# Kernel tuning notes

Hardware: AMD Instinct MI355X
Metric: run time of the kernel (lower is better)

Reference implementation:

```python
import jax, jax.numpy as jnp
import numpy as np

LAYERS, DIM, FFN, HEADS = 2, 1024, 4096, 8
HD = DIM // HEADS          # head qk dim = 128
VD = DIM                   # v_dim (double_v_dim=False)
HV = VD // HEADS           # head v dim = 128
B, L = 2, 2048
SCALE_BASE = 512.0
EPS = 1e-5


def setup_inputs() -> dict:
    key = jax.random.key(0)
    ks = jax.random.split(key, 18)
    def rn(k, shape, s=1.0):
        return jax.random.normal(k, shape, dtype=jnp.float32) * s
    return dict(
        X=rn(ks[0], (B, L, DIM)),
        Wq=rn(ks[1], (LAYERS, HEADS, DIM, HD), 1.0 / DIM),
        Wk=rn(ks[2], (LAYERS, HEADS, DIM, HD), 1.0 / DIM),
        Wv=rn(ks[3], (LAYERS, HEADS, DIM, HV), 1.0 / DIM),
        W_G=rn(ks[4], (LAYERS, DIM, VD), 1.0 / DIM),
        W_O=rn(ks[5], (LAYERS, VD, DIM), 1.0 / DIM),
        gn_w=1.0 + 0.02 * rn(ks[6], (LAYERS, VD)),
        gn_b=0.02 * rn(ks[7], (LAYERS, VD)),
        ln1_w=1.0 + 0.02 * rn(ks[8], (LAYERS, DIM)),
        ln1_b=0.02 * rn(ks[9], (LAYERS, DIM)),
        ln2_w=1.0 + 0.02 * rn(ks[10], (LAYERS, DIM)),
        ln2_b=0.02 * rn(ks[11], (LAYERS, DIM)),
        ffn_w1=rn(ks[12], (LAYERS, DIM, FFN), DIM ** -0.5),
        ffn_b1=0.02 * rn(ks[13], (LAYERS, FFN)),
        ffn_w2=rn(ks[14], (LAYERS, FFN, DIM), FFN ** -0.5),
        ffn_b2=0.02 * rn(ks[15], (LAYERS, DIM)),
    )


def _xpos_tables(length, head_dim):
    half = head_dim // 2
    pos = jnp.arange(length, dtype=jnp.float32)
    base_scale = (jnp.arange(0, head_dim, 2, dtype=jnp.float32) + 0.4 * head_dim) / (1.4 * head_dim)
    sc = base_scale[None, :] ** (pos / SCALE_BASE)[:, None]          # [L, half]
    inv_freq = 1.0 / (10000.0 ** (jnp.arange(half, dtype=jnp.float32) / half))
    ang = pos[:, None] * inv_freq[None, :]                           # [L, half]
    return sc, jnp.sin(ang), jnp.cos(ang)


def _dup(t):
    # duplicate_interleave: [L, half] -> [L, head_dim]
    return jnp.repeat(t, 2, axis=-1)


def _rotate_every_two(x):
    x1, x2 = x[..., ::2], x[..., 1::2]
    return jnp.stack([-x2, x1], axis=-1).reshape(x.shape)


def _apply_xpos(x, sc, sin, cos, downscale):
    s = 1.0 / sc if downscale else sc
    return x * _dup(cos * s) + _rotate_every_two(x) * _dup(sin * s)


def _layernorm(x, w, b):
    mu = jnp.mean(x, axis=-1, keepdims=True)
    var = jnp.var(x, axis=-1, keepdims=True)
    return (x - mu) * jax.lax.rsqrt(var + EPS) * w + b


def _decay_matrix(length):
    gammas = jnp.asarray(1.0 - np.exp(np.linspace(np.log(1 / 32), np.log(1 / 512), HEADS)), dtype=jnp.float32)
    n = jnp.arange(length, dtype=jnp.float32)
    delta = n[:, None] - n[None, :]                                  # [L, L]
    logg = jnp.log(gammas)[:, None, None]                            # [H, 1, 1]
    return jnp.where(delta[None] >= 0, jnp.exp(logg * delta[None]), 0.0)  # [H, L, L]


def _msr(X, Wq, Wk, Wv, gn_w, gn_b, W_G, W_O, D, sc, sin, cos):
    b, l, d = X.shape
    Q = _apply_xpos(jnp.einsum('bld,hde->bhle', X, Wq), sc, sin, cos, False)
    K = _apply_xpos(jnp.einsum('bld,hde->bhle', X, Wk), sc, sin, cos, True)
    V = jnp.einsum('bld,hdv->bhlv', X, Wv)
    scores = jnp.einsum('bhle,bhme->bhlm', Q, K) * D[None]           # [B,H,L,L] decayed
    Y = jnp.einsum('bhlm,bhmv->bhlv', scores, V)                     # [B,H,L,HV]
    # GroupNorm(heads, v_dim) over per-token concatenated heads == per-head norm
    mu = jnp.mean(Y, axis=-1, keepdims=True)
    var = jnp.var(Y, axis=-1, keepdims=True)
    Yn = (Y - mu) * jax.lax.rsqrt(var + EPS)
    Yn = Yn * gn_w.reshape(HEADS, 1, HV)[None] + gn_b.reshape(HEADS, 1, HV)[None]
    Yc = jnp.transpose(Yn, (0, 2, 1, 3)).reshape(b, l, VD)
    G = X @ W_G
    gate = G * jax.nn.sigmoid(G)                                     # swish
    return (gate * Yc) @ W_O


def reference(X, Wq, Wk, Wv, W_G, W_O, gn_w, gn_b, ln1_w, ln1_b, ln2_w, ln2_b, ffn_w1, ffn_b1, ffn_w2, ffn_b2):
    l = X.shape[1]
    sc, sin, cos = _xpos_tables(l, HD)
    D = _decay_matrix(l)
    for i in range(LAYERS):
        Y = _msr(_layernorm(X, ln1_w[i], ln1_b[i]), Wq[i], Wk[i], Wv[i],
                 gn_w[i], gn_b[i], W_G[i], W_O[i], D, sc, sin, cos) + X
        h = _layernorm(Y, ln2_w[i], ln2_b[i])
        h = jax.nn.gelu(h @ ffn_w1[i] + ffn_b1[i], approximate=False)
        X = h @ ffn_w2[i] + ffn_b2[i] + Y                            # Dropout is identity in eval
    return X
```

## Files before the change

kernel.cpp:

```cpp
#include <hip/hip_runtime.h>
#include <math.h>

#define DIM 1024
#define FFN_DIM 4096
#define HEADS 8
#define HD 128
#define BB 2
#define LL 2048
#define NROWS (BB*LL)

typedef __attribute__((ext_vector_type(8))) short bf16x8;
typedef __attribute__((ext_vector_type(4))) short bf16x4;
typedef __attribute__((ext_vector_type(2))) short bf16x2;
typedef __attribute__((ext_vector_type(4))) float f32x4;

__device__ inline short f2bf(float f) {
    unsigned u = __builtin_bit_cast(unsigned, f);
    unsigned r = (u + 0x7FFFu + ((u >> 16) & 1u)) >> 16;
    return (short)r;
}
__device__ inline float bf2f(short s) {
    unsigned u = ((unsigned)(unsigned short)s) << 16;
    return __builtin_bit_cast(float, u);
}

__device__ __forceinline__ void gl_lds16(const void* g, void* l) {
    __builtin_amdgcn_global_load_lds(
        (const __attribute__((address_space(1))) unsigned int*)g,
        (__attribute__((address_space(3))) unsigned int*)l, 16, 0, 0);
}

__global__ __launch_bounds__(256) void ln_kernel_bf(
    const float* __restrict__ x, const float* __restrict__ w,
    const float* __restrict__ b, short* __restrict__ out)
{
    int row = blockIdx.x;
    int tid = threadIdx.x;
    const float* xr = x + (size_t)row * DIM;
    float4 v = *(const float4*)(xr + tid * 4);
    float s  = v.x + v.y + v.z + v.w;
    float ss = v.x*v.x + v.y*v.y + v.z*v.z + v.w*v.w;
    #pragma unroll
    for (int o = 32; o > 0; o >>= 1) { s += __shfl_down(s, o); ss += __shfl_down(ss, o); }
    __shared__ float red[10];
    int wid = tid >> 6;
    if ((tid & 63) == 0) { red[wid] = s; red[4 + wid] = ss; }
    __syncthreads();
    if (tid == 0) {
        float t  = red[0] + red[1] + red[2] + red[3];
        float t2 = red[4] + red[5] + red[6] + red[7];
        float mu  = t * (1.f / DIM);
        float var = t2 * (1.f / DIM) - mu * mu;
        red[8] = mu; red[9] = rsqrtf(var + 1e-5f);
    }
    __syncthreads();
    float mu = red[8], rs = red[9];
    float4 wv = *(const float4*)(w + tid * 4);
    float4 bv = *(const float4*)(b + tid * 4);
    bf16x4 o;
    o[0] = f2bf((v.x - mu) * rs * wv.x + bv.x);
    o[1] = f2bf((v.y - mu) * rs * wv.y + bv.y);
    o[2] = f2bf((v.z - mu) * rs * wv.z + bv.z);
    o[3] = f2bf((v.w - mu) * rs * wv.w + bv.w);
    *(bf16x4*)(out + (size_t)row * DIM + tid * 4) = o;
}

__global__ __launch_bounds__(256) void transpose_cvt(
    const float* __restrict__ in, short* __restrict__ out,
    int R, int C, size_t ibs, size_t obs)
{
    __shared__ float t[32][33];
    int bz = blockIdx.z;
    int r0 = blockIdx.y * 32, c0 = blockIdx.x * 32;
    int tx = threadIdx.x & 31, ty = threadIdx.x >> 5;
    const float* ip = in + (size_t)bz * ibs;
    short* op = out + (size_t)bz * obs;
    #pragma unroll
    for (int i = 0; i < 4; ++i)
        t[ty + i * 8][tx] = ip[(size_t)(r0 + ty + i * 8) * C + c0 + tx];
    __syncthreads();
    #pragma unroll
    for (int i = 0; i < 4; ++i)
        op[(size_t)(c0 + ty + i * 8) * R + r0 + tx] = f2bf(t[tx][ty + i * 8]);
}

__global__ __launch_bounds__(256) void vt_cvt(
    const short* __restrict__ Vb, short* __restrict__ Vt)
{
    __shared__ short t[32][34];
    int r0 = blockIdx.y * 32, c0 = blockIdx.x * 32;
    int tx = threadIdx.x & 31, ty = threadIdx.x >> 5;
    #pragma unroll
    for (int i = 0; i < 4; ++i)
        t[ty + i * 8][tx] = Vb[(size_t)(r0 + ty + i * 8) * DIM + c0 + tx];
    __syncthreads();
    int b = r0 >> 11;
    int l = (r0 & (LL - 1));
    #pragma unroll
    for (int i = 0; i < 4; ++i) {
        int c = c0 + ty + i * 8;
        int h = c >> 7, v = c & 127;
        Vt[(((size_t)(b * HEADS + h) * HD + v) << 11) + l + tx] = t[tx][ty + i * 8];
    }
}

template<int EPI, int MI, int NI, int GX>
__global__ __launch_bounds__(512, 2) void gemm_pipe(
    const short* __restrict__ A, const short* __restrict__ Bt,
    void* __restrict__ Cv, const float* __restrict__ bias,
    const float* __restrict__ R_,
    void* __restrict__ P1, void* __restrict__ P2, void* __restrict__ P3,
    int N, int K, int M)
{
    constexpr int BM = 32 * MI;
    constexpr int BN = 64 * NI;
    constexpr int NBUF = (MI == 4) ? 4 : 2;
    __shared__ __align__(16) short As[NBUF][BM * 64];
    __shared__ __align__(16) short Bs[NBUF][BN * 64];
    int tid = threadIdx.x;
    int w = tid >> 6, lane = tid & 63;
    int q = lane >> 4, lr = lane & 15;
    int wr = w >> 2, wc = w & 3;

    int id = blockIdx.y * GX + blockIdx.x;
    int xcd = id & 7, j = id >> 3;
    constexpr int rx_n = (GX >= 8) ? GX / 8 : 1;
    int tp = (GX * gridDim.y) >> 3;
    int rh = tp >> 3;
    int lbx = j & 7, lby = j >> 3;
    int rx = xcd % rx_n, ry = xcd / rx_n;
    int bm = (ry * rh + lby) * BM;
    int bn = (rx * 8 + lbx) * BN;

    f32x4 acc[MI][NI];
    #pragma unroll
    for (int mi = 0; mi < MI; ++mi)
        #pragma unroll
        for (int ni = 0; ni < NI; ++ni) acc[mi][ni] = (f32x4){0.f, 0.f, 0.f, 0.f};

    int nk = K >> 6;

    if constexpr (MI == 8) {
        int segoff = (q ^ ((lr >> 1) & 3)) << 3;

        auto stageAh = [&](int bb, int kglob, int kh) {
            #pragma unroll
            for (int i = 0; i < 2; ++i) {
                int c = i * 512 + tid;
                int row = c >> 2, seg = c & 3;
                gl_lds16(A + (size_t)(bm + row) * K + kglob + ((seg ^ ((row >> 1) & 3)) << 3),
                         &As[bb][kh * 8192 + c * 8]);
            }
        };
        auto stageBh = [&](int bb, int kglob, int kh) {
            #pragma unroll
            for (int i = 0; i < 2; ++i) {
                int c = i * 512 + tid;
                int row = c >> 2, seg = c & 3;
                gl_lds16(Bt + (size_t)(bn + row) * K + kglob + ((seg ^ ((row >> 1) & 3)) << 3),
                         &Bs[bb][kh * 8192 + c * 8]);
            }
        };
        auto ldA = [&](int b, int kh, int ma, bf16x8* af) {
            #pragma unroll
            for (int mi = 0; mi < 4; ++mi)
                af[mi] = *(const bf16x8*)&As[b][kh * 8192 +
                         (wr * 128 + ma * 64 + mi * 16 + lr) * 32 + segoff];
        };
        auto ldB = [&](int b, int kh, bf16x8* bq) {
            #pragma unroll
            for (int ni = 0; ni < 4; ++ni)
                bq[ni] = *(const bf16x8*)&Bs[b][kh * 8192 +
                         (wc * 64 + ni * 16 + lr) * 32 + segoff];
        };

        stageAh(0, 0, 0); stageBh(0, 0, 0); stageAh(0, 32, 1); stageBh(0, 32, 1);
        asm volatile("s_waitcnt vmcnt(4)\ns_barrier" ::: "memory");

        #pragma unroll 1
        for (int kt = 0; kt < nk; ++kt) {
            int b = kt & 1;
            int kn = (kt + 1) << 6;
            bool pf = (kt + 1 < nk);
            bf16x8 af[4], bq[4];
            ldB(b, 0, bq); ldA(b, 0, 0, af);
            if (pf) stageAh(b ^ 1, kn, 0);
            asm volatile("s_barrier" ::: "memory");
            __builtin_amdgcn_s_setprio(1);
            #pragma unroll
            for (int mi = 0; mi < 4; ++mi)
                #pragma unroll
                for (int ni = 0; ni < 4; ++ni)
                    acc[mi][ni] = __builtin_amdgcn_mfma_f32_16x16x32_bf16(af[mi], bq[ni], acc[mi][ni], 0, 0, 0);
            __builtin_amdgcn_s_setprio(0);
            asm volatile("s_barrier" ::: "memory");
            ldA(b, 0, 1, af);
            if (pf) stageBh(b ^ 1, kn, 0);
            asm volatile("s_barrier" ::: "memory");
            __builtin_amdgcn_s_setprio(1);
            #pragma unroll
            for (int mi = 0; mi < 4; ++mi)
                #pragma unroll
                for (int ni = 0; ni < 4; ++ni)
                    acc[4 + mi][ni] = __builtin_amdgcn_mfma_f32_16x16x32_bf16(af[mi], bq[ni], acc[4 + mi][ni], 0, 0, 0);
            __builtin_amdgcn_s_setprio(0);
            if (pf) asm volatile("s_waitcnt vmcnt(4)\ns_barrier" ::: "memory");
            else    asm volatile("s_waitcnt vmcnt(0)\ns_barrier" ::: "memory");
            ldB(b, 1, bq); ldA(b, 1, 0, af);
            if (pf) stageAh(b ^ 1, kn + 32, 1);
            asm volatile("s_barrier" ::: "memory");
            __builtin_amdgcn_s_setprio(1);
            #pragma unroll
            for (int mi = 0; mi < 4; ++mi)
                #pragma unroll
                for (int ni = 0; ni < 4; ++ni)
                    acc[mi][ni] = __builtin_amdgcn_mfma_f32_16x16x32_bf16(af[mi], bq[ni], acc[mi][ni], 0, 0, 0);
            __builtin_amdgcn_s_setprio(0);
            asm volatile("s_barrier" ::: "memory");
            ldA(b, 1, 1, af);
            if (pf) stageBh(b ^ 1, kn + 32, 1);
            asm volatile("s_barrier" ::: "memory");
            __builtin_amdgcn_s_setprio(1);
            #pragma unroll
            for (int mi = 0; mi < 4; ++mi)
                #pragma unroll
                for (int ni = 0; ni < 4; ++ni)
                    acc[4 + mi][ni] = __builtin_amdgcn_mfma_f32_16x16x32_bf16(af[mi], bq[ni], acc[4 + mi][ni], 0, 0, 0);
            __builtin_amdgcn_s_setprio(0);
            if (pf) asm volatile("s_waitcnt vmcnt(4)\ns_barrier" ::: "memory");
            else    asm volatile("s_barrier" ::: "memory");
        }
    } else {
        int srow = tid >> 3;
        int sseg = tid & 7;
        auto stageA = [&](int bb, int k0) {
            #pragma unroll
            for (int i = 0; i < BM / 64; ++i) {
                int row = i * 64 + srow;
                gl_lds16(A + (size_t)(bm + row) * K + k0 + ((sseg ^ (row & 7)) << 3),
                         &As[bb][(i * 512 + tid) * 8]);
            }
        };
        auto stageB = [&](int bb, int k0) {
            #pragma unroll
            for (int i = 0; i < BN / 64; ++i) {
                int row = i * 64 + srow;
                gl_lds16(Bt + (size_t)(bn + row) * K + k0 + ((sseg ^ (row & 7)) << 3),
                         &Bs[bb][(i * 512 + tid) * 8]);
            }
        };
        int aoff = (wr * (BM / 2) + lr) * 64;
        int boff = (wc * (BN / 4) + lr) * 64;
        int seg0 = ((q ^ (lr & 7)) << 3);
        int seg1 = (((4 + q) ^ (lr & 7)) << 3);
        auto compute_half = [&](const short* as, const short* bs, int seg) {
            bf16x8 af[MI], bfr[NI];
            #pragma unroll
            for (int mi = 0; mi < MI; ++mi)
                af[mi] = *(const bf16x8*)&as[aoff + mi * 1024 + seg];
            #pragma unroll
            for (int ni = 0; ni < NI; ++ni)
                bfr[ni] = *(const bf16x8*)&bs[boff + ni * 1024 + seg];
            __builtin_amdgcn_s_setprio(1);
            #pragma unroll
            for (int mi = 0; mi < MI; ++mi)
                #pragma unroll
                for (int ni = 0; ni < NI; ++ni)
                    acc[mi][ni] = __builtin_amdgcn_mfma_f32_16x16x32_bf16(af[mi], bfr[ni], acc[mi][ni], 0, 0, 0);
            __builtin_amdgcn_s_setprio(0);
        };

        #pragma unroll
        for (int d = 0; d < 3; ++d) {
            stageA(d, d << 6);
            stageB(d, d << 6);
        }
        #pragma unroll 1
        for (int kt = 0; kt < nk; ++kt) {
            int b = kt & 3;
            if (kt + 3 < nk) {
                int bb = (kt + 3) & 3;
                stageA(bb, (kt + 3) << 6);
                stageB(bb, (kt + 3) << 6);
            }
            int rem = nk - 1 - kt;
            if (rem >= 3)      asm volatile("s_waitcnt vmcnt(12)\ns_barrier" ::: "memory");
            else if (rem == 2) asm volatile("s_waitcnt vmcnt(8)\ns_barrier" ::: "memory");
            else if (rem == 1) asm volatile("s_waitcnt vmcnt(4)\ns_barrier" ::: "memory");
            else               asm volatile("s_waitcnt vmcnt(0)\ns_barrier" ::: "memory");
            compute_half(As[b], Bs[b], seg0);
            compute_half(As[b], Bs[b], seg1);
            asm volatile("s_barrier" ::: "memory");
        }
    }

    if constexpr (EPI == 4) {
        int sel = bn >> 10;
        int row_base = bm + wr * (BM / 2) + q * 4;
        int l0 = row_base & (LL - 1);
        #pragma unroll
        for (int ni = 0; ni < NI; ++ni) {
            int col = bn + wc * (BN / 4) + ni * 16 + lr;
            int cq = col & (DIM - 1);
            if (sel <= 1) {
                int jj = (col & 127) >> 1;
                float lb = log2f((2.f * jj + 51.2f) / 179.2f);
                if (sel == 1) lb = -lb;
                float invf = exp2f(-(float)jj * (13.287712379549449f / 64.f));
                float snb, cnb;
                sincosf((float)l0 * invf, &snb, &cnb);
                float scb = exp2f(lb * (float)l0 * (1.f / 512.f));
                float s1, c1, s16, c16;
                __sincosf(invf, &s1, &c1);
                __sincosf(16.f * invf, &s16, &c16);
                float st1 = exp2f(lb * (1.f / 512.f));
                float st16 = exp2f(lb * (16.f / 512.f));
                short* Ob = (short*)(sel == 0 ? Cv : P1);
                #pragma unroll
                for (int mi = 0; mi < MI; ++mi) {
                    float cr = cnb, sr = snb, sv = scb;
                    #pragma unroll
                    for (int r = 0; r < 4; ++r) {
                        float cs = cr * sv, ssn = sr * sv;
                        float v = acc[mi][ni][r];
                        float p = __shfl_xor(v, 1);
                        float o = (lr & 1) ? (v * cs + p * ssn) : (v * cs - p * ssn);
                        Ob[(size_t)(row_base + mi * 16 + r) * DIM + cq] = f2bf(o);
                        if (r < 3) {
                            float crn = cr * c1 - sr * s1;
                            sr = sr * c1 + cr * s1; cr = crn;
                            sv *= st1;
                        }
                    }
                    float cbn = cnb * c16 - snb * s16;
                    snb = snb * c16 + cnb * s16; cnb = cbn;
                    scb *= st16;
                }
            } else if (sel == 2) {
                short* Vb = (short*)P2;
                #pragma unroll
                for (int mi = 0; mi < MI; ++mi)
                    #pragma unroll
                    for (int r = 0; r < 4; ++r)
                        Vb[(size_t)(row_base + mi * 16 + r) * DIM + cq] = f2bf(acc[mi][ni][r]);
            } else {
                short* Gb = (short*)P3;
                #pragma unroll
                for (int mi = 0; mi < MI; ++mi)
                    #pragma unroll
                    for (int r = 0; r < 4; ++r)
                        Gb[(size_t)(row_base + mi * 16 + r) * DIM + cq] = f2bf(acc[mi][ni][r]);
            }
        }
        return;
    }

    float* Cf = (float*)Cv;
    short* Cs = (short*)Cv;
    #pragma unroll
    for (int ni = 0; ni < NI; ++ni) {
        int col = bn + wc * (BN / 4) + ni * 16 + lr;
        float bi = 0.f;
        if constexpr (EPI == 1 || EPI == 2) bi = bias[col];
        #pragma unroll
        for (int mi = 0; mi < MI; ++mi) {
            int row0 = bm + wr * (BM / 2) + mi * 16 + q * 4;
            #pragma unroll
            for (int r = 0; r < 4; ++r) {
                size_t off = (size_t)(row0 + r) * M + col;
                float v = acc[mi][ni][r];
                if constexpr (EPI == 1) {
                    v += bi;
                    v = 0.5f * v * (1.f + erff(v * 0.70710678118654752f));
                    Cs[off] = f2bf(v);
                } else if constexpr (EPI == 2) {
                    Cf[off] = v + bi + R_[off];
                } else if constexpr (EPI == 3) {
                    Cf[off] = v + R_[off];
                } else {
                    Cf[off] = v;
                }
            }
        }
    }
}

#define PSTR 40
__global__ __launch_bounds__(512, 2) void retention_mfma2(
    const short* __restrict__ Qb, const short* __restrict__ Kb,
    const short* __restrict__ Vt, float* __restrict__ Y)
{
    __shared__ __align__(16) short Ks[2][64 * 128];
    __shared__ __align__(16) short Vs[2][128 * 64];
    __shared__ __align__(16) short Ps[8][16 * PSTR];
    int tid = threadIdx.x;
    int w = tid >> 6, lane = tid & 63;
    int q = lane >> 4, lr = lane & 15;
    int g = w >> 2;
    int qw = w & 3;
    int bh = blockIdx.x;
    int b = bh >> 3, h = bh & 7;
    size_t bL = (size_t)b * LL;
    const short* Kbh = Kb + (bL << 10) + (h << 7);
    const short* Qbh = Qb + (bL << 10) + (h << 7);
    const short* Vbh = Vt + ((size_t)bh << 18);
    float* Ybh = Y + (bL << 10) + (h << 7);

    const float lg_lo = -3.4657359027997265f;
    const float lg_hi = -6.2383246250395075f;
    float gamma = 1.f - expf(lg_lo + (lg_hi - lg_lo) * ((float)h / 7.f));
    float logg = logf(gamma);
    float gm64 = expf(-64.f * logg);
    float rf[4];
    #pragma unroll
    for (int r = 0; r < 4; ++r) rf[r] = expf(logg * (float)(q * 4 + r));
    float cf0 = expf(-logg * (float)lr);
    float cf1 = expf(-logg * (float)(16 + lr));
    int dqlr = q * 4 - lr;

    int kr_l = lane >> 4;
    int ks_l = lane & 15;
    int vr_l = lane >> 3;
    int vs_l = lane & 7;

    auto stageKV = [&](int bb, int m0) {
        #pragma unroll
        for (int i = 0; i < 2; ++i) {
            int ch = w * 2 + i;
            int kr = ch * 4 + kr_l;
            gl_lds16(Kbh + ((size_t)(m0 + kr) << 10) + ((ks_l ^ (kr & 15)) << 3),
                     &Ks[bb][ch * 512]);
            int vr = ch * 8 + vr_l;
            gl_lds16(Vbh + ((size_t)vr << 11) + m0 + ((vs_l ^ (vr & 7)) << 3),
                     &Vs[bb][ch * 512]);
        }
    };

    #pragma unroll 1
    for (int pass = 0; pass < 2; ++pass) {
        int jt = pass ? (31 - blockIdx.y) : blockIdx.y;
        int l0w = jt * 64 + qw * 16;
        int ns = jt + 1;

        bf16x8 qf[4];
        {
            const short* qp = Qbh + ((size_t)(l0w + lr) << 10) + q * 8;
            #pragma unroll
            for (int es = 0; es < 4; ++es) qf[es] = *(const bf16x8*)(qp + es * 32);
        }
        f32x4 yacc[8];
        #pragma unroll
        for (int vt = 0; vt < 8; ++vt) yacc[vt] = (f32x4){0.f, 0.f, 0.f, 0.f};
        float tf = expf(logg * (float)(l0w - g * 32));

        stageKV(0, 0);

        #pragma unroll 1
        for (int s = 0; s < ns; ++s) {
            int buf = s & 1;
            if (s + 1 < ns) {
                stageKV(buf ^ 1, (s + 1) * 64);
                asm volatile("s_waitcnt vmcnt(4)\ns_barrier" ::: "memory");
            } else {
                asm volatile("s_waitcnt vmcnt(0)\ns_barrier" ::: "memory");
            }
            int m0 = s * 64 + g * 32;
            if (m0 <= l0w + 15) {
                int dt = l0w - m0;
                const short* ksub = &Ks[buf][g * 32 * 128];
                f32x4 sa0 = (f32x4){0.f,0.f,0.f,0.f};
                f32x4 sa1 = (f32x4){0.f,0.f,0.f,0.f};
                #pragma unroll
                for (int es = 0; es < 4; ++es) {
                    int slot = ((es * 4 + q) ^ lr) * 8;
                    bf16x8 bk0 = *(const bf16x8*)&ksub[lr * 128 + slot];
                    bf16x8 bk1 = *(const bf16x8*)&ksub[(16 + lr) * 128 + slot];
                    sa0 = __builtin_amdgcn_mfma_f32_16x16x32_bf16(qf[es], bk0, sa0, 0, 0, 0);
                    sa1 = __builtin_amdgcn_mfma_f32_16x16x32_bf16(qf[es], bk1, sa1, 0, 0, 0);
                }
                #pragma unroll
                for (int r = 0; r < 4; ++r) {
                    float p0 = sa0[r] * (rf[r] * cf0 * tf);
                    float p1 = sa1[r] * (rf[r] * cf1 * tf);
                    int d0 = dt + dqlr + r;
                    Ps[w][(q*4 + r) * PSTR + lr]      = (d0 >= 0)      ? f2bf(p0) : (short)0;
                    Ps[w][(q*4 + r) * PSTR + 16 + lr] = (d0 - 16 >= 0) ? f2bf(p1) : (short)0;
                }
                bf16x8 pa = *(const bf16x8*)&Ps[w][lr * PSTR + q * 8];
                #pragma unroll
                for (int vt = 0; vt < 8; ++vt) {
                    bf16x8 bv = *(const bf16x8*)&Vs[buf][(vt * 16 + lr) * 64 + (((g * 4 + q) ^ (lr & 7)) << 3)];
                    yacc[vt] = __builtin_amdgcn_mfma_f32_16x16x32_bf16(pa, bv, yacc[vt], 0, 0, 0);
                }
            }
            tf *= gm64;
            asm volatile("s_barrier" ::: "memory");
        }
        __syncthreads();
        float* sc = (float*)&Ks[0][0] + qw * 2048;
        if (g) {
            #pragma unroll
            for (int vt = 0; vt < 8; ++vt)
                #pragma unroll
                for (int r = 0; r < 4; ++r)
                    sc[(q * 4 + r) * 128 + ((vt * 16 + lr) ^ (q * 8))] = yacc[vt][r];
        }
        __syncthreads();
        if (!g) {
            float* yp = Ybh + ((size_t)(l0w + q * 4) << 10) + lr;
            #pragma unroll
            for (int vt = 0; vt < 8; ++vt)
                #pragma unroll
                for (int r = 0; r < 4; ++r)
                    yp[((size_t)r << 10) + vt * 16] =
                        yacc[vt][r] + sc[(q * 4 + r) * 128 + ((vt * 16 + lr) ^ (q * 8))];
        }
        __syncthreads();
    }
}

__global__ __launch_bounds__(256) void gn_gate_kernel(
    const float* __restrict__ Y, const short* __restrict__ Gb,
    const float* __restrict__ w, const float* __restrict__ b,
    short* __restrict__ ybf)
{
    int tid = threadIdx.x;
    int wid = tid >> 6, lane = tid & 63;
    int grp = blockIdx.x * 4 + wid;
    int n = grp >> 3, h = grp & 7;
    size_t base = (size_t)n * DIM + h * HD + lane * 2;
    float2 y = *(const float2*)(Y + base);
    float s = y.x + y.y, ss = y.x * y.x + y.y * y.y;
    #pragma unroll
    for (int o = 32; o > 0; o >>= 1) { s += __shfl_down(s, o); ss += __shfl_down(ss, o); }
    s = __shfl(s, 0); ss = __shfl(ss, 0);
    float mu  = s * (1.f / HD);
    float var = ss * (1.f / HD) - mu * mu;
    float rs  = rsqrtf(var + 1e-5f);
    float2 wv = *(const float2*)(w + h * HD + lane * 2);
    float2 bv = *(const float2*)(b + h * HD + lane * 2);
    bf16x2 gv = *(const bf16x2*)(Gb + base);
    float gx = bf2f(gv[0]), gy = bf2f(gv[1]);
    float g0 = gx / (1.f + expf(-gx));
    float g1 = gy / (1.f + expf(-gy));
    bf16x2 o;
    o[0] = f2bf(((y.x - mu) * rs * wv.x + bv.x) * g0);
    o[1] = f2bf(((y.y - mu) * rs * wv.y + bv.y) * g1);
    *(bf16x2*)(ybf + base) = o;
}

extern "C" void kernel_launch(void* const* d_in, const int* in_sizes, int n_in,
                              void* d_out, int out_size, void* d_ws, size_t ws_size,
                              hipStream_t stream)
{
    const float* X0   = (const float*)d_in[0];
    const float* Wq   = (const float*)d_in[1];
    const float* Wk   = (const float*)d_in[2];
    const float* Wv   = (const float*)d_in[3];
    const float* WG   = (const float*)d_in[4];
    const float* WO   = (const float*)d_in[5];
    const float* gnw  = (const float*)d_in[6];
    const float* gnb  = (const float*)d_in[7];
    const float* ln1w = (const float*)d_in[8];
    const float* ln1b = (const float*)d_in[9];
    const float* ln2w = (const float*)d_in[10];
    const float* ln2b = (const float*)d_in[11];
    const float* fw1  = (const float*)d_in[12];
    const float* fb1  = (const float*)d_in[13];
    const float* fw2  = (const float*)d_in[14];
    const float* fb2  = (const float*)d_in[15];

    float* ws = (float*)d_ws;
    const size_t U = (size_t)NROWS * DIM;

    short* lnbf  = (short*)(ws + 0 * U);
    short* wqkvg = lnbf + (size_t)NROWS * DIM;
    short* Vt   = (short*)(ws + 1 * U);
    short* fw1t = (short*)(ws + 1 * U);
    short* fw2t = fw1t + (size_t)DIM * FFN_DIM;
    float* sY  = ws + 2 * U;
    short* h1   = (short*)(ws + 2 * U);
    short* Vb   = (short*)(ws + 3 * U);
    short* ybf  = (short*)(ws + 3 * U);
    short* wot  = ybf + (size_t)NROWS * DIM;
    short* Gb   = (short*)(ws + 4 * U);
    float* sXn = ws + 4 * U;
    short* Qb   = (short*)(ws + 5 * U);
    short* Kb   = Qb + (size_t)NROWS * DIM;
    float* sX  = ws + 6 * U;

    for (int i = 0; i < 2; ++i) {
        const float* Xin = (i == 0) ? X0 : sX;
        float* Xout = (i == 1) ? (float*)d_out : sX;

        ln_kernel_bf<<<NROWS, 256, 0, stream>>>(Xin, ln1w + i * DIM, ln1b + i * DIM, lnbf);
        dim3 tq(HD / 32, DIM / 32, HEADS);
        transpose_cvt<<<tq, 256, 0, stream>>>(Wq + (size_t)i * HEADS * DIM * HD, wqkvg + 0 * DIM * DIM, DIM, HD, (size_t)DIM * HD, (size_t)HD * DIM);
        transpose_cvt<<<tq, 256, 0, stream>>>(Wk + (size_t)i * HEADS * DIM * HD, wqkvg + 1 * DIM * DIM, DIM, HD, (size_t)DIM * HD, (size_t)HD * DIM);
        transpose_cvt<<<tq, 256, 0, stream>>>(Wv + (size_t)i * HEADS * DIM * HD, wqkvg + 2 * DIM * DIM, DIM, HD, (size_t)DIM * HD, (size_t)HD * DIM);
        dim3 tg(DIM / 32, DIM / 32, 1);
        transpose_cvt<<<tg, 256, 0, stream>>>(WG + (size_t)i * DIM * DIM, wqkvg + 3 * (size_t)DIM * DIM, DIM, DIM, 0, 0);
        dim3 gp4(4 * DIM / 256, NROWS / 256);
        gemm_pipe<4, 8, 4, 16><<<gp4, 512, 0, stream>>>(lnbf, wqkvg, Qb, nullptr, nullptr, Kb, Vb, Gb, NROWS, DIM, 4 * DIM);
        dim3 vg(DIM / 32, NROWS / 32);
        vt_cvt<<<vg, 256, 0, stream>>>(Vb, Vt);
        dim3 rg(16, 16);
        retention_mfma2<<<rg, 512, 0, stream>>>(Qb, Kb, Vt, sY);
        gn_gate_kernel<<<NROWS * HEADS / 4, 256, 0, stream>>>(sY, Gb, gnw + i * DIM, gnb + i * DIM, ybf);
        transpose_cvt<<<tg, 256, 0, stream>>>(WO + (size_t)i * DIM * DIM, wot, DIM, DIM, 0, 0);
        dim3 gp(DIM / 128, NROWS / 128);
        gemm_pipe<3, 4, 2, 8><<<gp, 512, 0, stream>>>(ybf, wot, sXn, nullptr, Xin, nullptr, nullptr, nullptr, NROWS, DIM, DIM);
        ln_kernel_bf<<<NROWS, 256, 0, stream>>>(sXn, ln2w + i * DIM, ln2b + i * DIM, lnbf);
        dim3 t1(FFN_DIM / 32, DIM / 32, 1);
        transpose_cvt<<<t1, 256, 0, stream>>>(fw1 + (size_t)i * DIM * FFN_DIM, fw1t, DIM, FFN_DIM, 0, 0);
        dim3 t2(DIM / 32, FFN_DIM / 32, 1);
        transpose_cvt<<<t2, 256, 0, stream>>>(fw2 + (size_t)i * FFN_DIM * DIM, fw2t, FFN_DIM, DIM, 0, 0);
        dim3 gf1(FFN_DIM / 256, NROWS / 256);
        gemm_pipe<1, 8, 4, 16><<<gf1, 512, 0, stream>>>(lnbf, fw1t, h1, fb1 + i * FFN_DIM, nullptr, nullptr, nullptr, nullptr, NROWS, DIM, FFN_DIM);
        dim3 gf2(DIM / 128, NROWS / 128);
        gemm_pipe<2, 4, 2, 8><<<gf2, 512, 0, stream>>>(h1, fw2t, Xout, fb2 + i * DIM, sXn, nullptr, nullptr, nullptr, NROWS, FFN_DIM, DIM);
    }
}
```

Measured before the change: 725.8 us.

## Precompute xPos rotary tables and manually unroll double-buffered GEMM k-loop

Adds a small kernel that precomputes per-position, per-frequency xPos cos/sin times scale tables for Q (upscaled) and K (downscaled) into workspace. The QKVG GEMM epilogue now loads these tables instead of evaluating transcendental functions and running recurrences per thread. It also unrolls the pipelined k-loop by two so the buffer index is a compile-time constant. This trades epilogue ALU work for an extra launch and scattered global table reads. The unroll assumes nk is even.

```diff
diff --git a/kernel.cpp b/kernel.cpp
--- a/kernel.cpp
+++ b/kernel.cpp
@@ -28,6 +28,21 @@
     __builtin_amdgcn_global_load_lds(
         (const __attribute__((address_space(1))) unsigned int*)g,
         (__attribute__((address_space(3))) unsigned int*)l, 16, 0, 0);
+}
+
+__global__ __launch_bounds__(256) void xpos_tables(float2* __restrict__ tq,
+                                                   float2* __restrict__ tk)
+{
+    int idx = blockIdx.x * 256 + threadIdx.x;
+    int j = idx & 63, l = idx >> 6;
+    float lb = log2f((2.f * j + 51.2f) / 179.2f);
+    float invf = exp2f(-(float)j * (13.287712379549449f / 64.f));
+    float s, c;
+    sincosf((float)l * invf, &s, &c);
+    float scu = exp2f(lb * (float)l * (1.f / 512.f));
+    float scd = exp2f(-lb * (float)l * (1.f / 512.f));
+    tq[idx] = make_float2(c * scu, s * scu);
+    tk[idx] = make_float2(c * scd, s * scd);
 }
 
 __global__ __launch_bounds__(256) void ln_kernel_bf(
@@ -174,12 +189,7 @@
                          (wc * 64 + ni * 16 + lr) * 32 + segoff];
         };
 
-        stageAh(0, 0, 0); stageBh(0, 0, 0); stageAh(0, 32, 1); stageBh(0, 32, 1);
-        asm volatile("s_waitcnt vmcnt(4)\ns_barrier" ::: "memory");
-
-        #pragma unroll 1
-        for (int kt = 0; kt < nk; ++kt) {
-            int b = kt & 1;
+        auto tile_body = [&](int b, int kt) {
             int kn = (kt + 1) << 6;
             bool pf = (kt + 1 < nk);
             bf16x8 af[4], bq[4];
@@ -229,6 +239,15 @@
             __builtin_amdgcn_s_setprio(0);
             if (pf) asm volatile("s_waitcnt vmcnt(4)\ns_barrier" ::: "memory");
             else    asm volatile("s_barrier" ::: "memory");
+        };
+
+        stageAh(0, 0, 0); stageBh(0, 0, 0); stageAh(0, 32, 1); stageBh(0, 32, 1);
+        asm volatile("s_waitcnt vmcnt(4)\ns_barrier" ::: "memory");
+
+        #pragma unroll 1
+        for (int kt = 0; kt < nk; kt += 2) {
+            tile_body(0, kt);
+            tile_body(1, kt + 1);
         }
     } else {
         int srow = tid >> 3;
@@ -298,43 +317,25 @@
         int sel = bn >> 10;
         int row_base = bm + wr * (BM / 2) + q * 4;
         int l0 = row_base & (LL - 1);
+        const float2* tbl = (const float2*)(sel == 0 ? bias : R_);
         #pragma unroll
         for (int ni = 0; ni < NI; ++ni) {
             int col = bn + wc * (BN / 4) + ni * 16 + lr;
             int cq = col & (DIM - 1);
             if (sel <= 1) {
                 int jj = (col & 127) >> 1;
-                float lb = log2f((2.f * jj + 51.2f) / 179.2f);
-                if (sel == 1) lb = -lb;
-                float invf = exp2f(-(float)jj * (13.287712379549449f / 64.f));
-                float snb, cnb;
-                sincosf((float)l0 * invf, &snb, &cnb);
-                float scb = exp2f(lb * (float)l0 * (1.f / 512.f));
-                float s1, c1, s16, c16;
-                __sincosf(invf, &s1, &c1);
-                __sincosf(16.f * invf, &s16, &c16);
-                float st1 = exp2f(lb * (1.f / 512.f));
-                float st16 = exp2f(lb * (16.f / 512.f));
                 short* Ob = (short*)(sel == 0 ? Cv : P1);
                 #pragma unroll
                 for (int mi = 0; mi < MI; ++mi) {
-                    float cr = cnb, sr = snb, sv = scb;
                     #pragma unroll
                     for (int r = 0; r < 4; ++r) {
-                        float cs = cr * sv, ssn = sr * sv;
+                        int l = l0 + mi * 16 + r;
+                        float2 t = tbl[((size_t)l << 6) + jj];
                         float v = acc[mi][ni][r];
                         float p = __shfl_xor(v, 1);
-                        float o = (lr & 1) ? (v * cs + p * ssn) : (v * cs - p * ssn);
+                        float o = (lr & 1) ? (v * t.x + p * t.y) : (v * t.x - p * t.y);
                         Ob[(size_t)(row_base + mi * 16 + r) * DIM + cq] = f2bf(o);
-                        if (r < 3) {
-                            float crn = cr * c1 - sr * s1;
-                            sr = sr * c1 + cr * s1; cr = crn;
-                            sv *= st1;
-                        }
                     }
-                    float cbn = cnb * c16 - snb * s16;
-                    snb = snb * c16 + cnb * s16; cnb = cbn;
-                    scb *= st16;
                 }
             } else if (sel == 2) {
                 short* Vb = (short*)P2;
@@ -588,6 +589,8 @@
     short* Qb   = (short*)(ws + 5 * U);
     short* Kb   = Qb + (size_t)NROWS * DIM;
     float* sX  = ws + 6 * U;
+    float2* tqg = (float2*)(ws + 2 * U);
+    float2* tkg = tqg + (size_t)LL * 64;
 
     for (int i = 0; i < 2; ++i) {
         const float* Xin = (i == 0) ? X0 : sX;
@@ -600,8 +603,9 @@
         transpose_cvt<<<tq, 256, 0, stream>>>(Wv + (size_t)i * HEADS * DIM * HD, wqkvg + 2 * DIM * DIM, DIM, HD, (size_t)DIM * HD, (size_t)HD * DIM);
         dim3 tg(DIM / 32, DIM / 32, 1);
         transpose_cvt<<<tg, 256, 0, stream>>>(WG + (size_t)i * DIM * DIM, wqkvg + 3 * (size_t)DIM * DIM, DIM, DIM, 0, 0);
+        xpos_tables<<<LL * 64 / 256, 256, 0, stream>>>(tqg, tkg);
         dim3 gp4(4 * DIM / 256, NROWS / 256);
-        gemm_pipe<4, 8, 4, 16><<<gp4, 512, 0, stream>>>(lnbf, wqkvg, Qb, nullptr, nullptr, Kb, Vb, Gb, NROWS, DIM, 4 * DIM);
+        gemm_pipe<4, 8, 4, 16><<<gp4, 512, 0, stream>>>(lnbf, wqkvg, Qb, (const float*)tqg, (const float*)tkg, Kb, Vb, Gb, NROWS, DIM, 4 * DIM);
         dim3 vg(DIM / 32, NROWS / 32);
         vt_cvt<<<vg, 256, 0, stream>>>(Vb, Vt);
         dim3 rg(16, 16);
```

Result: no change. 718.2 us (-1.0%).
